# Kernel optimization log

Hardware: AMD Instinct MI355X
Metric: run time of the kernel (lower is better)

The kernel has to match this reference:

```python
import jax, jax.numpy as jnp
from jax import lax
import numpy as np

E = 512        # embedding_dim (= rnn_first hidden, conv kernel, pool kernel)
VOCAB = 50000
H = 512        # hidden_dim of rnn_second
TEMP = 256     # Double_Linear out_feature
NL = 2         # num_layers (rnn_first layers == conv channels == second seq len)
NE = 2         # num_epoches (outer loop in forward)
T = 256        # sentence length
OUT = 1        # out_dim
PAD = (E - 1) // 2                       # 255
CONV_OUT = (E + 2 * PAD - (E - 1) - 1) // 2 + 1   # 256
POOL_OUT = (CONV_OUT + 2 * PAD - (E - 1) - 1) // 2 + 1  # 128 = rnn_second input


def _gru_scan(gi_all, h0, Whh, bhh):
    """PyTorch-convention GRU over precomputed input gates gi_all [T, 3H]."""
    def step(h, gi):
        gh = h @ Whh.T + bhh
        ir, iz, inn = jnp.split(gi, 3)
        hr, hz, hnn = jnp.split(gh, 3)
        r = jax.nn.sigmoid(ir + hr)
        z = jax.nn.sigmoid(iz + hz)
        n = jnp.tanh(inn + r * hnn)
        hn = (1.0 - z) * n + z * h
        return hn, hn
    return lax.scan(step, h0, gi_all)


def setup_inputs() -> dict:
    key = jax.random.key(0)
    ks = jax.random.split(key, 20)
    s = 0.05
    f32 = jnp.float32
    return {
        "sentA": jax.random.randint(ks[0], (T,), 0, VOCAB),
        "sentB": jax.random.randint(ks[1], (T,), 0, VOCAB),
        "emb": jax.random.normal(ks[2], (VOCAB, E), f32),
        "Wih1": jax.random.normal(ks[3], (NL, 3 * E, E), f32) * s,
        "Whh1": jax.random.normal(ks[4], (NL, 3 * E, E), f32) * s,
        "bih1": jax.random.normal(ks[5], (NL, 3 * E), f32) * s,
        "bhh1": jax.random.normal(ks[6], (NL, 3 * E), f32) * s,
        "conv_w": jax.random.normal(ks[7], (NL, NL, E), f32) * s,
        "conv_b": jax.random.normal(ks[8], (NL,), f32) * s,
        "Wih2": jax.random.normal(ks[9], (3 * H, POOL_OUT), f32) * s,
        "Whh2": jax.random.normal(ks[10], (3 * H, H), f32) * s,
        "bih2": jax.random.normal(ks[11], (3 * H,), f32) * s,
        "bhh2": jax.random.normal(ks[12], (3 * H,), f32) * s,
        "WA": jax.random.normal(ks[13], (H, TEMP), f32) * s,
        "WB": jax.random.normal(ks[14], (H, TEMP), f32) * s,
        "b_bi": jax.random.normal(ks[15], (TEMP,), f32) * s,
        "W_lin": jax.random.normal(ks[16], (OUT, TEMP), f32) * s,
        "b_lin": jax.random.normal(ks[17], (OUT,), f32) * s,
    }


def reference(sentA, sentB, emb, Wih1, Whh1, bih1, bhh1, conv_w, conv_b,
              Wih2, Whh2, bih2, bhh2, WA, WB, b_bi, W_lin, b_lin):
    dt = emb.dtype

    def encode(sent):
        h = emb[sent]                                   # [L, E]
        for _ in range(NE):                             # num_epoches loop
            x = h
            finals = []
            for l in range(NL):                         # stacked GRU layers
                gi = x @ Wih1[l].T + bih1[l]            # [L, 3E]
                hT, x = _gru_scan(gi, jnp.zeros((E,), dt), Whh1[l], bhh1[l])
                finals.append(hT)
            h = jnp.stack(finals)                       # hn: [NL, E] -> next seq
        # conv1d (in=out=NL channels, kernel E, stride 2) + maxpool1d
        y = lax.conv_general_dilated(h[None], conv_w, (2,), [(PAD, PAD)],
                                     dimension_numbers=("NCH", "OIH", "NCH"))
        y = y + conv_b[None, :, None]                   # [1, NL, CONV_OUT]
        y = lax.reduce_window(y, -jnp.inf, lax.max, (1, 1, E), (1, 1, 2),
                              [(0, 0), (0, 0), (PAD, PAD)])
        seq = y[0]                                      # [NL, POOL_OUT]
        gi2 = seq @ Wih2.T + bih2                       # [NL, 3H]
        hT, _ = _gru_scan(gi2, jnp.zeros((H,), dt), Whh2, bhh2)
        return hT                                       # [H]

    hA = encode(sentA)
    hB = encode(sentB)
    hx = hA * hB
    hv = jnp.abs(hA - hB)
    hs = hx @ WA + hv @ WB + b_bi                       # Double_Linear
    ht = jnp.tanh(hs)
    out = jax.nn.sigmoid(ht @ W_lin.T + b_lin)
    return out[None]                                    # [1, OUT]
```

## Files before the change

### kernel.cpp

```cpp
#include <hip/hip_runtime.h>
#include <math.h>


__device__ __forceinline__ float sigm(float x) { return 1.f / (1.f + expf(-x)); }

#define POISON_U32 0x40000000u

#define LDSP(k) ((k) + (((k) >> 4) << 2))

__device__ __forceinline__ float red32(float v) {
    v += __shfl_xor(v, 16, 64);
    v += __shfl_xor(v, 8, 64);
    v += __shfl_xor(v, 4, 64);
    v += __shfl_xor(v, 2, 64);
    v += __shfl_xor(v, 1, 64);
    return v;
}

__device__ __forceinline__ void poll_ge(const unsigned int* p, unsigned tgt) {
    unsigned v;
    do {
        v = __hip_atomic_load(p, __ATOMIC_RELAXED, __HIP_MEMORY_SCOPE_AGENT);
        if (v < tgt) __builtin_amdgcn_s_sleep(1);
    } while (v < tgt);
}

__device__ __forceinline__ void stage4_poison(float* dstbase, const float* src,
                                              int idx) {
    const unsigned long long* sp = (const unsigned long long*)src + idx * 2;
    unsigned long long d0, d1;
    for (;;) {
        d0 = __hip_atomic_load(sp + 0, __ATOMIC_RELAXED, __HIP_MEMORY_SCOPE_AGENT);
        d1 = __hip_atomic_load(sp + 1, __ATOMIC_RELAXED, __HIP_MEMORY_SCOPE_AGENT);
        if ((unsigned)(d0 & 0xFFFFFFFFu) != POISON_U32 &&
            (unsigned)(d0 >> 32)         != POISON_U32 &&
            (unsigned)(d1 & 0xFFFFFFFFu) != POISON_U32 &&
            (unsigned)(d1 >> 32)         != POISON_U32) break;
        __builtin_amdgcn_s_sleep(1);
    }
    union { unsigned long long u; float2 f; } c0, c1;
    c0.u = d0; c1.u = d1;
    float* d = dstbase + LDSP(idx * 4);
    d[0] = c0.f.x; d[1] = c0.f.y; d[2] = c1.f.x; d[3] = c1.f.y;
}

__device__ __forceinline__ void stage1024(float* dst, const float* src, int tid) {
    if (tid < 256) {
        const unsigned long long* s = (const unsigned long long*)src + tid * 2;
        unsigned long long d0 = __hip_atomic_load(s + 0, __ATOMIC_RELAXED,
                                                  __HIP_MEMORY_SCOPE_AGENT);
        unsigned long long d1 = __hip_atomic_load(s + 1, __ATOMIC_RELAXED,
                                                  __HIP_MEMORY_SCOPE_AGENT);
        union { unsigned long long u; float2 f; } c0, c1;
        c0.u = d0; c1.u = d1;
        float* d = dst + LDSP(tid * 4);
        d[0] = c0.f.x; d[1] = c0.f.y; d[2] = c1.f.x; d[3] = c1.f.y;
    }
}

__device__ __forceinline__ float gru1(float gr, float gz, float gn,
                                      float ar, float az, float an,
                                      const float bh[3], float hp) {
    float r = sigm(gr + ar + bh[0]);
    float z = sigm(gz + az + bh[1]);
    float n = tanhf(gn + r * (an + bh[2]));
    return (1.f - z) * n + z * hp;
}

__global__ __launch_bounds__(512, 1) void k_pipe(
    const float* __restrict__ Whh1, const float* __restrict__ bhh1,
    const float* __restrict__ Wih1, const float* __restrict__ bih1,
    const float* __restrict__ emb,
    const int* __restrict__ sentA, const int* __restrict__ sentB,
    float* __restrict__ e2x,
    float* __restrict__ hbuf0,
    float* __restrict__ hbuf1)
{
    const int tid   = threadIdx.x;
    const int layer = blockIdx.x >> 5;
    const int wgi   = blockIdx.x & 31;
    const int grp   = tid >> 5;
    const int lane  = tid & 31;
    const int j     = wgi * 16 + grp;
    const int colbase = lane * 16;

    __shared__ float xl[2][1280];
    __shared__ float hl[2][1280];

    const size_t WS = (size_t)1536 * 512;
    const float* WH = Whh1 + (size_t)layer * WS;
    const float* WI = Wih1 + (size_t)layer * WS;

    float wh[3][16], wi[3][16];
#pragma unroll
    for (int q = 0; q < 3; ++q) {
        const float* srcH = WH + (size_t)(q * 512 + j) * 512 + colbase;
        const float* srcI = WI + (size_t)(q * 512 + j) * 512 + colbase;
#pragma unroll
        for (int c4 = 0; c4 < 4; ++c4) {
            float4 vH = *(const float4*)(srcH + c4 * 4);
            float4 vI = *(const float4*)(srcI + c4 * 4);
            wh[q][c4*4+0] = vH.x; wh[q][c4*4+1] = vH.y;
            wh[q][c4*4+2] = vH.z; wh[q][c4*4+3] = vH.w;
            wi[q][c4*4+0] = vI.x; wi[q][c4*4+1] = vI.y;
            wi[q][c4*4+2] = vI.z; wi[q][c4*4+3] = vI.w;
        }
    }
#pragma unroll
    for (int q = 0; q < 3; ++q)
#pragma unroll
        for (int c = 0; c < 16; ++c) {
            asm volatile("" : "+v"(wh[q][c]));
            asm volatile("" : "+v"(wi[q][c]));
        }

    float bh[3], bi[3];
#pragma unroll
    for (int q = 0; q < 3; ++q) {
        bh[q] = bhh1[layer * 1536 + q * 512 + j];
        bi[q] = bih1[layer * 1536 + q * 512 + j];
    }

    float* hout = (layer == 0) ? hbuf0 : hbuf1;
    float hprev[2] = {0.f, 0.f};

    for (int t = 1; t <= 256; ++t) {
        const int p = t & 1;

        if (tid < 256) {
            if (layer == 0) {
                const int i = tid * 4, s = i >> 9, k = i & 511;
                const int idx = s ? sentB[t - 1] : sentA[t - 1];
                float4 v = *(const float4*)(emb + (size_t)idx * 512 + k);
                float* d = &xl[p][LDSP(i)];
                d[0] = v.x; d[1] = v.y; d[2] = v.z; d[3] = v.w;
            } else {
                stage4_poison(xl[p], hbuf0 + (size_t)t * 1024, tid);
            }
        } else if (t > 1) {
            stage4_poison(hl[p], hout + (size_t)(t - 1) * 1024, tid - 256);
        }
        __syncthreads();

        float aR[2] = {0.f,0.f}, aZ[2] = {0.f,0.f};
        float aGN[2] = {0.f,0.f}, aHN[2] = {0.f,0.f};
#pragma unroll
        for (int s = 0; s < 2; ++s) {
            const int base = s * 640 + 20 * lane;
#pragma unroll
            for (int c4 = 0; c4 < 4; ++c4) {
                float4 xv = *(const float4*)&xl[p][base + c4 * 4];
                aR[s]  += wi[0][c4*4+0]*xv.x + wi[0][c4*4+1]*xv.y
                        + wi[0][c4*4+2]*xv.z + wi[0][c4*4+3]*xv.w;
                aZ[s]  += wi[1][c4*4+0]*xv.x + wi[1][c4*4+1]*xv.y
                        + wi[1][c4*4+2]*xv.z + wi[1][c4*4+3]*xv.w;
                aGN[s] += wi[2][c4*4+0]*xv.x + wi[2][c4*4+1]*xv.y
                        + wi[2][c4*4+2]*xv.z + wi[2][c4*4+3]*xv.w;
            }
            if (t > 1) {
#pragma unroll
                for (int c4 = 0; c4 < 4; ++c4) {
                    float4 hv = *(const float4*)&hl[p][base + c4 * 4];
                    aR[s]  += wh[0][c4*4+0]*hv.x + wh[0][c4*4+1]*hv.y
                            + wh[0][c4*4+2]*hv.z + wh[0][c4*4+3]*hv.w;
                    aZ[s]  += wh[1][c4*4+0]*hv.x + wh[1][c4*4+1]*hv.y
                            + wh[1][c4*4+2]*hv.z + wh[1][c4*4+3]*hv.w;
                    aHN[s] += wh[2][c4*4+0]*hv.x + wh[2][c4*4+1]*hv.y
                            + wh[2][c4*4+2]*hv.z + wh[2][c4*4+3]*hv.w;
                }
            }
        }
#pragma unroll
        for (int s = 0; s < 2; ++s) {
            aR[s] = red32(aR[s]); aZ[s] = red32(aZ[s]);
            aGN[s] = red32(aGN[s]); aHN[s] = red32(aHN[s]);
        }

        float hn[2];
#pragma unroll
        for (int s = 0; s < 2; ++s) {
            float r = sigm(aR[s] + bi[0] + bh[0]);
            float z = sigm(aZ[s] + bi[1] + bh[1]);
            float n = tanhf(aGN[s] + bi[2] + r * (aHN[s] + bh[2]));
            hn[s] = (1.f - z) * n + z * hprev[s];
            hprev[s] = hn[s];
        }

        if (lane == 0) {
#pragma unroll
            for (int s = 0; s < 2; ++s) {
                __hip_atomic_store(hout + (size_t)t * 1024 + s * 512 + j, hn[s],
                                   __ATOMIC_RELAXED, __HIP_MEMORY_SCOPE_AGENT);
                if (t == 256)
                    e2x[s * 1024 + layer * 512 + j] = hn[s];
            }
        }
    }
}

__global__ __launch_bounds__(512, 1) void k_tail(
    const float* __restrict__ Wih1, const float* __restrict__ bih1,
    const float* __restrict__ Whh1, const float* __restrict__ bhh1,
    const float* __restrict__ convw, const float* __restrict__ convb,
    const float* __restrict__ Whh2, const float* __restrict__ bhh2,
    const float* __restrict__ bih2, const float* __restrict__ Srow,
    const float* __restrict__ e2x,
    const float* __restrict__ WA, const float* __restrict__ WB,
    const float* __restrict__ b_bi, const float* __restrict__ Wlin,
    const float* __restrict__ blin,
    float* __restrict__ tb0, float* __restrict__ tb1, float* __restrict__ tr,
    float* __restrict__ Mmax,
    unsigned int* __restrict__ tctr, unsigned int* __restrict__ mf,
    float* __restrict__ outp)
{
    const int tid = threadIdx.x;
    const int wgi = blockIdx.x;
    const int grp = tid >> 5, lane = tid & 31;
    const int j = wgi * 16 + grp, colbase = lane * 16;
    const size_t WS = (size_t)1536 * 512;

    __shared__ float xlds[1280];
    __shared__ float hlds[1280];
    __shared__ float red[8];
    __shared__ float smax[4];

#define WAIT_ALL(val)  do { if (tid < 32) poll_ge(tctr + tid * 16, (unsigned)(val)); \
                            __syncthreads(); } while (0)
#define PUBLISH(val)   do { __builtin_amdgcn_s_waitcnt(0); __syncthreads(); \
                            if (tid == 0) __hip_atomic_store(tctr + wgi * 16, (unsigned)(val), \
                                __ATOMIC_RELAXED, __HIP_MEMORY_SCOPE_AGENT); } while (0)

    if (tid < 256) {
        const int i = tid * 4, s = i >> 9, k = i & 511;
        float4 v = *(const float4*)(e2x + s * 1024 + k);
        float* d = xlds + LDSP(i);
        d[0] = v.x; d[1] = v.y; d[2] = v.z; d[3] = v.w;
    } else {
        const int i = (tid - 256) * 4, s = i >> 9, k = i & 511;
        float4 v = *(const float4*)(e2x + s * 1024 + 512 + k);
        float* d = hlds + LDSP(i);
        d[0] = v.x; d[1] = v.y; d[2] = v.z; d[3] = v.w;
    }
    __syncthreads();

    float gp[2][2][3];
    float bh[3], hp[2];
#pragma unroll
    for (int q = 0; q < 3; ++q) {
        const float* wp = Wih1 + (size_t)(q * 512 + j) * 512 + colbase;
        float w16[16];
#pragma unroll
        for (int c4 = 0; c4 < 4; ++c4) {
            float4 v = *(const float4*)(wp + c4 * 4);
            w16[c4*4+0] = v.x; w16[c4*4+1] = v.y; w16[c4*4+2] = v.z; w16[c4*4+3] = v.w;
        }
        float d00 = 0.f, d01 = 0.f, d10 = 0.f, d11 = 0.f;
#pragma unroll
        for (int c4 = 0; c4 < 4; ++c4) {
            float4 x0 = *(const float4*)&xlds[0 * 640 + 20 * lane + c4 * 4];
            float4 x1 = *(const float4*)&xlds[1 * 640 + 20 * lane + c4 * 4];
            float4 y0 = *(const float4*)&hlds[0 * 640 + 20 * lane + c4 * 4];
            float4 y1 = *(const float4*)&hlds[1 * 640 + 20 * lane + c4 * 4];
            d00 += w16[c4*4+0]*x0.x + w16[c4*4+1]*x0.y + w16[c4*4+2]*x0.z + w16[c4*4+3]*x0.w;
            d01 += w16[c4*4+0]*x1.x + w16[c4*4+1]*x1.y + w16[c4*4+2]*x1.z + w16[c4*4+3]*x1.w;
            d10 += w16[c4*4+0]*y0.x + w16[c4*4+1]*y0.y + w16[c4*4+2]*y0.z + w16[c4*4+3]*y0.w;
            d11 += w16[c4*4+0]*y1.x + w16[c4*4+1]*y1.y + w16[c4*4+2]*y1.z + w16[c4*4+3]*y1.w;
        }
        const float biq = bih1[q * 512 + j];
        gp[0][0][q] = red32(d00) + biq; gp[0][1][q] = red32(d01) + biq;
        gp[1][0][q] = red32(d10) + biq; gp[1][1][q] = red32(d11) + biq;
    }
#pragma unroll
    for (int q = 0; q < 3; ++q) bh[q] = bhh1[q * 512 + j];

#pragma unroll
    for (int s = 0; s < 2; ++s)
        hp[s] = gru1(gp[0][s][0], gp[0][s][1], gp[0][s][2], 0.f, 0.f, 0.f, bh, 0.f);
    if (lane == 0)
#pragma unroll
        for (int s = 0; s < 2; ++s)
            __hip_atomic_store(tb0 + 1024 + s * 512 + j, hp[s],
                               __ATOMIC_RELAXED, __HIP_MEMORY_SCOPE_AGENT);
    PUBLISH(1);

    WAIT_ALL(1);
    stage1024(hlds, tb0 + 1024, tid);
    __syncthreads();
    {
        float wh3[3][16];
#pragma unroll
        for (int q = 0; q < 3; ++q) {
            const float* wp = Whh1 + (size_t)(q * 512 + j) * 512 + colbase;
#pragma unroll
            for (int c4 = 0; c4 < 4; ++c4) {
                float4 v = *(const float4*)(wp + c4 * 4);
                wh3[q][c4*4+0] = v.x; wh3[q][c4*4+1] = v.y;
                wh3[q][c4*4+2] = v.z; wh3[q][c4*4+3] = v.w;
            }
        }
        float acc[3][2] = {{0.f,0.f},{0.f,0.f},{0.f,0.f}};
#pragma unroll
        for (int s = 0; s < 2; ++s) {
            const int base = s * 640 + 20 * lane;
#pragma unroll
            for (int c4 = 0; c4 < 4; ++c4) {
                float4 hv = *(const float4*)&hlds[base + c4 * 4];
#pragma unroll
                for (int q = 0; q < 3; ++q)
                    acc[q][s] += wh3[q][c4*4+0]*hv.x + wh3[q][c4*4+1]*hv.y
                               + wh3[q][c4*4+2]*hv.z + wh3[q][c4*4+3]*hv.w;
            }
        }
#pragma unroll
        for (int s = 0; s < 2; ++s) {
            float a0 = red32(acc[0][s]), a1 = red32(acc[1][s]), a2 = red32(acc[2][s]);
            hp[s] = gru1(gp[1][s][0], gp[1][s][1], gp[1][s][2], a0, a1, a2, bh, hp[s]);
        }
        if (lane == 0)
#pragma unroll
            for (int s = 0; s < 2; ++s)
                __hip_atomic_store(tb0 + 2048 + s * 512 + j, hp[s],
                                   __ATOMIC_RELAXED, __HIP_MEMORY_SCOPE_AGENT);
        PUBLISH(2);
    }

    WAIT_ALL(2);
    stage1024(xlds, tb0 + 1024, tid);
    if (tid >= 256) {
        const int i = tid - 256;
        const unsigned long long* s = (const unsigned long long*)(tb0 + 2048) + i * 2;
        unsigned long long d0 = __hip_atomic_load(s + 0, __ATOMIC_RELAXED, __HIP_MEMORY_SCOPE_AGENT);
        unsigned long long d1 = __hip_atomic_load(s + 1, __ATOMIC_RELAXED, __HIP_MEMORY_SCOPE_AGENT);
        union { unsigned long long u; float2 f; } c0, c1; c0.u = d0; c1.u = d1;
        float* d = hlds + LDSP(i * 4);
        d[0] = c0.f.x; d[1] = c0.f.y; d[2] = c1.f.x; d[3] = c1.f.y;
    }
    __syncthreads();
#pragma unroll
    for (int q = 0; q < 3; ++q) {
        const float* wp = Wih1 + WS + (size_t)(q * 512 + j) * 512 + colbase;
        float w16[16];
#pragma unroll
        for (int c4 = 0; c4 < 4; ++c4) {
            float4 v = *(const float4*)(wp + c4 * 4);
            w16[c4*4+0] = v.x; w16[c4*4+1] = v.y; w16[c4*4+2] = v.z; w16[c4*4+3] = v.w;
        }
        float d00 = 0.f, d01 = 0.f, d10 = 0.f, d11 = 0.f;
#pragma unroll
        for (int c4 = 0; c4 < 4; ++c4) {
            float4 x0 = *(const float4*)&xlds[0 * 640 + 20 * lane + c4 * 4];
            float4 x1 = *(const float4*)&xlds[1 * 640 + 20 * lane + c4 * 4];
            float4 y0 = *(const float4*)&hlds[0 * 640 + 20 * lane + c4 * 4];
            float4 y1 = *(const float4*)&hlds[1 * 640 + 20 * lane + c4 * 4];
            d00 += w16[c4*4+0]*x0.x + w16[c4*4+1]*x0.y + w16[c4*4+2]*x0.z + w16[c4*4+3]*x0.w;
            d01 += w16[c4*4+0]*x1.x + w16[c4*4+1]*x1.y + w16[c4*4+2]*x1.z + w16[c4*4+3]*x1.w;
            d10 += w16[c4*4+0]*y0.x + w16[c4*4+1]*y0.y + w16[c4*4+2]*y0.z + w16[c4*4+3]*y0.w;
            d11 += w16[c4*4+0]*y1.x + w16[c4*4+1]*y1.y + w16[c4*4+2]*y1.z + w16[c4*4+3]*y1.w;
        }
        const float biq = bih1[1536 + q * 512 + j];
        gp[0][0][q] = red32(d00) + biq; gp[0][1][q] = red32(d01) + biq;
        gp[1][0][q] = red32(d10) + biq; gp[1][1][q] = red32(d11) + biq;
    }
#pragma unroll
    for (int q = 0; q < 3; ++q) bh[q] = bhh1[1536 + q * 512 + j];

#pragma unroll
    for (int s = 0; s < 2; ++s)
        hp[s] = gru1(gp[0][s][0], gp[0][s][1], gp[0][s][2], 0.f, 0.f, 0.f, bh, 0.f);
    if (lane == 0)
#pragma unroll
        for (int s = 0; s < 2; ++s)
            __hip_atomic_store(tb1 + 1024 + s * 512 + j, hp[s],
                               __ATOMIC_RELAXED, __HIP_MEMORY_SCOPE_AGENT);
    PUBLISH(3);

    WAIT_ALL(3);
    stage1024(hlds, tb1 + 1024, tid);
    __syncthreads();
    {
        float wh3[3][16];
#pragma unroll
        for (int q = 0; q < 3; ++q) {
            const float* wp = Whh1 + WS + (size_t)(q * 512 + j) * 512 + colbase;
#pragma unroll
            for (int c4 = 0; c4 < 4; ++c4) {
                float4 v = *(const float4*)(wp + c4 * 4);
                wh3[q][c4*4+0] = v.x; wh3[q][c4*4+1] = v.y;
                wh3[q][c4*4+2] = v.z; wh3[q][c4*4+3] = v.w;
            }
        }
        float acc[3][2] = {{0.f,0.f},{0.f,0.f},{0.f,0.f}};
#pragma unroll
        for (int s = 0; s < 2; ++s) {
            const int base = s * 640 + 20 * lane;
#pragma unroll
            for (int c4 = 0; c4 < 4; ++c4) {
                float4 hv = *(const float4*)&hlds[base + c4 * 4];
#pragma unroll
                for (int q = 0; q < 3; ++q)
                    acc[q][s] += wh3[q][c4*4+0]*hv.x + wh3[q][c4*4+1]*hv.y
                               + wh3[q][c4*4+2]*hv.z + wh3[q][c4*4+3]*hv.w;
            }
        }
#pragma unroll
        for (int s = 0; s < 2; ++s) {
            float a0 = red32(acc[0][s]), a1 = red32(acc[1][s]), a2 = red32(acc[2][s]);
            hp[s] = gru1(gp[1][s][0], gp[1][s][1], gp[1][s][2], a0, a1, a2, bh, hp[s]);
        }
        if (lane == 0)
#pragma unroll
            for (int s = 0; s < 2; ++s)
                __hip_atomic_store(tb1 + 2048 + s * 512 + j, hp[s],
                                   __ATOMIC_RELAXED, __HIP_MEMORY_SCOPE_AGENT);
        PUBLISH(4);
    }

    WAIT_ALL(4);
    float m4[4];
    if (wgi == 0) {
        stage1024(xlds, tb0 + 2048, tid);
        if (tid >= 256) {
            const int i = tid - 256;
            const unsigned long long* s = (const unsigned long long*)(tb1 + 2048) + i * 2;
            unsigned long long d0 = __hip_atomic_load(s + 0, __ATOMIC_RELAXED, __HIP_MEMORY_SCOPE_AGENT);
            unsigned long long d1 = __hip_atomic_load(s + 1, __ATOMIC_RELAXED, __HIP_MEMORY_SCOPE_AGENT);
            union { unsigned long long u; float2 f; } c0, c1; c0.u = d0; c1.u = d1;
            float* d = hlds + LDSP(i * 4);
            d[0] = c0.f.x; d[1] = c0.f.y; d[2] = c1.f.x; d[3] = c1.f.y;
        }
        __syncthreads();
        for (int so = 0; so < 4; ++so) {
            const int s = so >> 1, o = so & 1;
            float acc = -3.4e38f;
            if (tid < 256) {
                acc = convb[o];
                const int base = 2 * tid - 255;
                for (int k = 0; k < 512; ++k) {
                    const int pos = base + k;
                    if ((unsigned)pos < 512u) {
                        const int gi0i = s * 512 + pos;
                        acc += xlds[LDSP(gi0i)] * convw[(size_t)(o * 2 + 0) * 512 + k]
                             + hlds[LDSP(gi0i)] * convw[(size_t)(o * 2 + 1) * 512 + k];
                    }
                }
            }
            float m = acc;
            m = fmaxf(m, __shfl_xor(m, 32, 64));
            m = fmaxf(m, __shfl_xor(m, 16, 64));
            m = fmaxf(m, __shfl_xor(m, 8, 64));
            m = fmaxf(m, __shfl_xor(m, 4, 64));
            m = fmaxf(m, __shfl_xor(m, 2, 64));
            m = fmaxf(m, __shfl_xor(m, 1, 64));
            if ((tid & 63) == 0) red[tid >> 6] = m;
            __syncthreads();
            if (tid == 0) {
                float mm = red[0];
                for (int i = 1; i < 8; ++i) mm = fmaxf(mm, red[i]);
                smax[so] = mm;
            }
            __syncthreads();
        }
        if (tid == 0) {
            for (int i = 0; i < 4; ++i)
                __hip_atomic_store(Mmax + i, smax[i],
                                   __ATOMIC_RELAXED, __HIP_MEMORY_SCOPE_AGENT);
            __builtin_amdgcn_s_waitcnt(0);
            __hip_atomic_store(mf, 1u, __ATOMIC_RELAXED, __HIP_MEMORY_SCOPE_AGENT);
        }
        __syncthreads();
#pragma unroll
        for (int i = 0; i < 4; ++i) m4[i] = smax[i];
    } else {
        if (tid == 0) poll_ge(mf, 1u);
        __syncthreads();
#pragma unroll
        for (int i = 0; i < 4; ++i)
            m4[i] = __hip_atomic_load((const float*)Mmax + i, __ATOMIC_RELAXED,
                                      __HIP_MEMORY_SCOPE_AGENT);
    }

    {
        float wh3[3][16];
#pragma unroll
        for (int q = 0; q < 3; ++q) {
            const float* wp = Whh2 + (size_t)(q * 512 + j) * 512 + colbase;
#pragma unroll
            for (int c4 = 0; c4 < 4; ++c4) {
                float4 v = *(const float4*)(wp + c4 * 4);
                wh3[q][c4*4+0] = v.x; wh3[q][c4*4+1] = v.y;
                wh3[q][c4*4+2] = v.z; wh3[q][c4*4+3] = v.w;
            }
        }
#pragma unroll
        for (int q = 0; q < 3; ++q) {
            const float sq = Srow[q * 512 + j];
            const float biq = bih2[q * 512 + j];
#pragma unroll
            for (int s = 0; s < 2; ++s) {
                gp[0][s][q] = m4[s * 2 + 0] * sq + biq;
                gp[1][s][q] = m4[s * 2 + 1] * sq + biq;
            }
            bh[q] = bhh2[q * 512 + j];
        }
#pragma unroll
        for (int s = 0; s < 2; ++s)
            hp[s] = gru1(gp[0][s][0], gp[0][s][1], gp[0][s][2], 0.f, 0.f, 0.f, bh, 0.f);
        if (lane == 0)
#pragma unroll
            for (int s = 0; s < 2; ++s)
                __hip_atomic_store(tr + 1024 + s * 512 + j, hp[s],
                                   __ATOMIC_RELAXED, __HIP_MEMORY_SCOPE_AGENT);
        PUBLISH(5);

        WAIT_ALL(5);
        stage1024(hlds, tr + 1024, tid);
        __syncthreads();
        float acc[3][2] = {{0.f,0.f},{0.f,0.f},{0.f,0.f}};
#pragma unroll
        for (int s = 0; s < 2; ++s) {
            const int base = s * 640 + 20 * lane;
#pragma unroll
            for (int c4 = 0; c4 < 4; ++c4) {
                float4 hv = *(const float4*)&hlds[base + c4 * 4];
#pragma unroll
                for (int q = 0; q < 3; ++q)
                    acc[q][s] += wh3[q][c4*4+0]*hv.x + wh3[q][c4*4+1]*hv.y
                               + wh3[q][c4*4+2]*hv.z + wh3[q][c4*4+3]*hv.w;
            }
        }
#pragma unroll
        for (int s = 0; s < 2; ++s) {
            float a0 = red32(acc[0][s]), a1 = red32(acc[1][s]), a2 = red32(acc[2][s]);
            hp[s] = gru1(gp[1][s][0], gp[1][s][1], gp[1][s][2], a0, a1, a2, bh, hp[s]);
        }
        if (lane == 0)
#pragma unroll
            for (int s = 0; s < 2; ++s)
                __hip_atomic_store(tr + 2048 + s * 512 + j, hp[s],
                                   __ATOMIC_RELAXED, __HIP_MEMORY_SCOPE_AGENT);
        PUBLISH(6);
    }

    WAIT_ALL(6);
    if (wgi != 0) return;
    stage1024(xlds, tr + 2048, tid);
    __syncthreads();
    float v = 0.f;
    if (tid < 256) {
        float acc = b_bi[tid];
        for (int jj = 0; jj < 512; ++jj) {
            const float a = xlds[LDSP(jj)];
            const float b = xlds[LDSP(512 + jj)];
            acc += (a * b) * WA[(size_t)jj * 256 + tid]
                 + fabsf(a - b) * WB[(size_t)jj * 256 + tid];
        }
        v = tanhf(acc) * Wlin[tid];
    }
    v += __shfl_xor(v, 32, 64);
    v += __shfl_xor(v, 16, 64);
    v += __shfl_xor(v, 8, 64);
    v += __shfl_xor(v, 4, 64);
    v += __shfl_xor(v, 2, 64);
    v += __shfl_xor(v, 1, 64);
    if ((tid & 63) == 0) red[tid >> 6] = v;
    __syncthreads();
    if (tid == 0) {
        float ssum = blin[0];
        for (int i = 0; i < 8; ++i) ssum += red[i];
        outp[0] = 1.f / (1.f + expf(-ssum));
    }
#undef WAIT_ALL
#undef PUBLISH
}

__global__ __launch_bounds__(256) void k_init(
    const float* __restrict__ Wih2, float* __restrict__ Srow,
    unsigned int* __restrict__ hbufs,
    unsigned int* __restrict__ flags)
{
    const int g = blockIdx.x * 256 + threadIdx.x;
    if (g < 1536) {
        float s = 0.f;
        for (int k = 0; k < 128; ++k) s += Wih2[(size_t)g * 128 + k];
        Srow[g] = s;
    }
    const int NBIG = 257 * 1024;
    const int NTOT = 2 * NBIG;
    for (int i = g; i < NTOT; i += gridDim.x * 256) {
        const int off = (i < NBIG) ? i : i - NBIG;
        hbufs[i] = (off < 1024) ? 0u : POISON_U32;
    }
    if (g < 528) flags[g] = 0u;
}

extern "C" void kernel_launch(void* const* d_in, const int* in_sizes, int n_in,
                              void* d_out, int out_size, void* d_ws, size_t ws_size,
                              hipStream_t stream)
{
    const int*   sentA = (const int*)d_in[0];
    const int*   sentB = (const int*)d_in[1];
    const float* emb   = (const float*)d_in[2];
    const float* Wih1  = (const float*)d_in[3];
    const float* Whh1  = (const float*)d_in[4];
    const float* bih1  = (const float*)d_in[5];
    const float* bhh1  = (const float*)d_in[6];
    const float* convw = (const float*)d_in[7];
    const float* convb = (const float*)d_in[8];
    const float* Wih2  = (const float*)d_in[9];
    const float* Whh2  = (const float*)d_in[10];
    const float* bih2  = (const float*)d_in[11];
    const float* bhh2  = (const float*)d_in[12];
    const float* WA    = (const float*)d_in[13];
    const float* WB    = (const float*)d_in[14];
    const float* b_bi  = (const float*)d_in[15];
    const float* Wlin  = (const float*)d_in[16];
    const float* blin  = (const float*)d_in[17];

    float* ws = (float*)d_ws;
    size_t off = 0;
    float* e2x    = ws + off; off += 2048;
    float* hbuf0  = ws + off; off += 257 * 1024;
    float* hbuf1  = ws + off; off += 257 * 1024;
    float* tb0    = ws + off; off += 3 * 1024;
    float* tb1    = ws + off; off += 3 * 1024;
    float* tr     = ws + off; off += 3 * 1024;
    float* Mmax   = ws + off; off += 16;
    float* Srow   = ws + off; off += 1536;
    unsigned int* flags = (unsigned int*)(ws + off);
    unsigned int* tctr = flags;
    unsigned int* mf   = flags + 512;

    k_init<<<256, 256, 0, stream>>>(Wih2, Srow, (unsigned int*)hbuf0, flags);

    k_pipe<<<64, 512, 0, stream>>>(Whh1, bhh1, Wih1, bih1, emb, sentA, sentB,
                                   e2x, hbuf0, hbuf1);

    k_tail<<<32, 512, 0, stream>>>(Wih1, bih1, Whh1, bhh1, convw, convb,
                                   Whh2, bhh2, bih2, Srow, e2x,
                                   WA, WB, b_bi, Wlin, blin,
                                   tb0, tb1, tr, Mmax, tctr, mf, (float*)d_out);
}
```

Before: 1.494 ms.

## Replace poison-value polling with per-workgroup step flags in GRU pipeline

The cross-workgroup handoff in the layer-1 GRU pipeline stops spinning on poison sentinels in the hidden-state buffers and instead polls per-workgroup step counters, each published after a waitcnt and barrier. This removes the init kernel's pass that poisoned roughly half a million words, so k_init shrinks to 8 blocks, and the Srow sum is vectorised. In exchange every timestep gains an extra barrier plus flag polling, double-buffered LDS becomes single-buffered, and correctness now depends on memory ordering between the relaxed data stores and the flag store.

```diff
diff --git a/kernel.cpp b/kernel.cpp
--- a/kernel.cpp
+++ b/kernel.cpp
@@ -3,8 +3,6 @@
 
 
 __device__ __forceinline__ float sigm(float x) { return 1.f / (1.f + expf(-x)); }
-
-#define POISON_U32 0x40000000u
 
 #define LDSP(k) ((k) + (((k) >> 4) << 2))
 
@@ -23,25 +21,6 @@
         v = __hip_atomic_load(p, __ATOMIC_RELAXED, __HIP_MEMORY_SCOPE_AGENT);
         if (v < tgt) __builtin_amdgcn_s_sleep(1);
     } while (v < tgt);
-}
-
-__device__ __forceinline__ void stage4_poison(float* dstbase, const float* src,
-                                              int idx) {
-    const unsigned long long* sp = (const unsigned long long*)src + idx * 2;
-    unsigned long long d0, d1;
-    for (;;) {
-        d0 = __hip_atomic_load(sp + 0, __ATOMIC_RELAXED, __HIP_MEMORY_SCOPE_AGENT);
-        d1 = __hip_atomic_load(sp + 1, __ATOMIC_RELAXED, __HIP_MEMORY_SCOPE_AGENT);
-        if ((unsigned)(d0 & 0xFFFFFFFFu) != POISON_U32 &&
-            (unsigned)(d0 >> 32)         != POISON_U32 &&
-            (unsigned)(d1 & 0xFFFFFFFFu) != POISON_U32 &&
-            (unsigned)(d1 >> 32)         != POISON_U32) break;
-        __builtin_amdgcn_s_sleep(1);
-    }
-    union { unsigned long long u; float2 f; } c0, c1;
-    c0.u = d0; c1.u = d1;
-    float* d = dstbase + LDSP(idx * 4);
-    d[0] = c0.f.x; d[1] = c0.f.y; d[2] = c1.f.x; d[3] = c1.f.y;
 }
 
 __device__ __forceinline__ void stage1024(float* dst, const float* src, int tid) {
@@ -74,7 +53,9 @@
     const int* __restrict__ sentA, const int* __restrict__ sentB,
     float* __restrict__ e2x,
     float* __restrict__ hbuf0,
-    float* __restrict__ hbuf1)
+    float* __restrict__ hbuf1,
+    unsigned int* __restrict__ fL0,
+    unsigned int* __restrict__ fL1)
 {
     const int tid   = threadIdx.x;
     const int layer = blockIdx.x >> 5;
@@ -84,8 +65,8 @@
     const int j     = wgi * 16 + grp;
     const int colbase = lane * 16;
 
-    __shared__ float xl[2][1280];
-    __shared__ float hl[2][1280];
+    __shared__ float xlds[1280];
+    __shared__ float hlds[1280];
 
     const size_t WS = (size_t)1536 * 512;
     const float* WH = Whh1 + (size_t)layer * WS;
@@ -122,23 +103,41 @@
     }
 
     float* hout = (layer == 0) ? hbuf0 : hbuf1;
+    unsigned int* myflag = ((layer == 0) ? fL0 : fL1) + wgi * 16;
     float hprev[2] = {0.f, 0.f};
 
     for (int t = 1; t <= 256; ++t) {
-        const int p = t & 1;
+        if (layer == 0) {
+            if (t > 1 && tid < 32) poll_ge(fL0 + tid * 16, (unsigned)(t - 1));
+        } else {
+            if (tid < 32) poll_ge(fL0 + tid * 16, (unsigned)t);
+            else if (t > 1 && tid >= 64 && tid < 96)
+                poll_ge(fL1 + (tid - 64) * 16, (unsigned)(t - 1));
+        }
+        __syncthreads();
 
         if (tid < 256) {
             if (layer == 0) {
                 const int i = tid * 4, s = i >> 9, k = i & 511;
                 const int idx = s ? sentB[t - 1] : sentA[t - 1];
                 float4 v = *(const float4*)(emb + (size_t)idx * 512 + k);
-                float* d = &xl[p][LDSP(i)];
+                float* d = &xlds[LDSP(i)];
                 d[0] = v.x; d[1] = v.y; d[2] = v.z; d[3] = v.w;
             } else {
-                stage4_poison(xl[p], hbuf0 + (size_t)t * 1024, tid);
+                stage1024(xlds, hbuf0 + (size_t)t * 1024, tid);
             }
         } else if (t > 1) {
-            stage4_poison(hl[p], hout + (size_t)(t - 1) * 1024, tid - 256);
+            const int i = tid - 256;
+            const unsigned long long* s =
+                (const unsigned long long*)(hout + (size_t)(t - 1) * 1024) + i * 2;
+            unsigned long long d0 = __hip_atomic_load(s + 0, __ATOMIC_RELAXED,
+                                                      __HIP_MEMORY_SCOPE_AGENT);
+            unsigned long long d1 = __hip_atomic_load(s + 1, __ATOMIC_RELAXED,
+                                                      __HIP_MEMORY_SCOPE_AGENT);
+            union { unsigned long long u; float2 f; } c0, c1;
+            c0.u = d0; c1.u = d1;
+            float* d = hlds + LDSP(i * 4);
+            d[0] = c0.f.x; d[1] = c0.f.y; d[2] = c1.f.x; d[3] = c1.f.y;
         }
         __syncthreads();
 
@@ -149,7 +148,7 @@
             const int base = s * 640 + 20 * lane;
 #pragma unroll
             for (int c4 = 0; c4 < 4; ++c4) {
-                float4 xv = *(const float4*)&xl[p][base + c4 * 4];
+                float4 xv = *(const float4*)&xlds[base + c4 * 4];
                 aR[s]  += wi[0][c4*4+0]*xv.x + wi[0][c4*4+1]*xv.y
                         + wi[0][c4*4+2]*xv.z + wi[0][c4*4+3]*xv.w;
                 aZ[s]  += wi[1][c4*4+0]*xv.x + wi[1][c4*4+1]*xv.y
@@ -160,7 +159,7 @@
             if (t > 1) {
 #pragma unroll
                 for (int c4 = 0; c4 < 4; ++c4) {
-                    float4 hv = *(const float4*)&hl[p][base + c4 * 4];
+                    float4 hv = *(const float4*)&hlds[base + c4 * 4];
                     aR[s]  += wh[0][c4*4+0]*hv.x + wh[0][c4*4+1]*hv.y
                             + wh[0][c4*4+2]*hv.z + wh[0][c4*4+3]*hv.w;
                     aZ[s]  += wh[1][c4*4+0]*hv.x + wh[1][c4*4+1]*hv.y
@@ -195,6 +194,11 @@
                     e2x[s * 1024 + layer * 512 + j] = hn[s];
             }
         }
+        __builtin_amdgcn_s_waitcnt(0);
+        __syncthreads();
+        if (tid == 0)
+            __hip_atomic_store(myflag, (unsigned)t,
+                               __ATOMIC_RELAXED, __HIP_MEMORY_SCOPE_AGENT);
     }
 }
 
@@ -575,22 +579,19 @@
 
 __global__ __launch_bounds__(256) void k_init(
     const float* __restrict__ Wih2, float* __restrict__ Srow,
-    unsigned int* __restrict__ hbufs,
     unsigned int* __restrict__ flags)
 {
     const int g = blockIdx.x * 256 + threadIdx.x;
     if (g < 1536) {
         float s = 0.f;
-        for (int k = 0; k < 128; ++k) s += Wih2[(size_t)g * 128 + k];
+        const float* row = Wih2 + (size_t)g * 128;
+        for (int k = 0; k < 128; k += 4) {
+            float4 v = *(const float4*)(row + k);
+            s += v.x + v.y + v.z + v.w;
+        }
         Srow[g] = s;
     }
-    const int NBIG = 257 * 1024;
-    const int NTOT = 2 * NBIG;
-    for (int i = g; i < NTOT; i += gridDim.x * 256) {
-        const int off = (i < NBIG) ? i : i - NBIG;
-        hbufs[i] = (off < 1024) ? 0u : POISON_U32;
-    }
-    if (g < 528) flags[g] = 0u;
+    if (g < 1552) flags[g] = 0u;
 }
 
 extern "C" void kernel_launch(void* const* d_in, const int* in_sizes, int n_in,
@@ -627,13 +628,15 @@
     float* Mmax   = ws + off; off += 16;
     float* Srow   = ws + off; off += 1536;
     unsigned int* flags = (unsigned int*)(ws + off);
-    unsigned int* tctr = flags;
-    unsigned int* mf   = flags + 512;
-
-    k_init<<<256, 256, 0, stream>>>(Wih2, Srow, (unsigned int*)hbuf0, flags);
+    unsigned int* fL0  = flags;
+    unsigned int* fL1  = flags + 512;
+    unsigned int* tctr = flags + 1024;
+    unsigned int* mf   = flags + 1536;
+
+    k_init<<<8, 256, 0, stream>>>(Wih2, Srow, flags);
 
     k_pipe<<<64, 512, 0, stream>>>(Whh1, bhh1, Wih1, bih1, emb, sentA, sentB,
-                                   e2x, hbuf0, hbuf1);
+                                   e2x, hbuf0, hbuf1, fL0, fL1);
 
     k_tail<<<32, 512, 0, stream>>>(Wih1, bih1, Whh1, bhh1, convw, convb,
                                    Whh2, bhh2, bih2, Srow, e2x,
```

Result: faster. 1.428 ms (-4.4%).
